# Optimization experiments

Measured on AMD Instinct MI355X. Metric: run time of the kernel, lower is better.

Reference implementation:

```python
import jax, jax.numpy as jnp
import numpy as np

N_NODES = 50000
N_EDGES = 800000
D_FEAT = 128
HIDDEN = 128
BERT_DIM = 768
BATCH = 4096
MAX_ENT = 20
COMB = BERT_DIM + HIDDEN  # 896


def setup_inputs() -> dict:
    key = jax.random.key(0)
    ks = jax.random.split(key, 12)
    article_bert_embeddings = jax.random.normal(ks[0], (BATCH, BERT_DIM), dtype=jnp.float32)
    x = jax.random.normal(ks[1], (N_NODES, D_FEAT), dtype=jnp.float32)
    edge_index = jax.random.randint(ks[2], (2, N_EDGES), 0, N_NODES, dtype=jnp.int64)
    entity_map = jax.random.randint(ks[3], (BATCH, MAX_ENT), 0, N_NODES, dtype=jnp.int64)
    pad = jax.random.uniform(ks[4], (BATCH, MAX_ENT)) < 0.3
    entity_map = jnp.where(pad, jnp.int64(-1), entity_map)
    s = 1.0 / np.sqrt(D_FEAT)
    W1 = jax.random.normal(ks[5], (D_FEAT, HIDDEN), dtype=jnp.float32) * s
    b1 = jnp.zeros((HIDDEN,), dtype=jnp.float32)
    W2 = jax.random.normal(ks[6], (HIDDEN, HIDDEN), dtype=jnp.float32) * (1.0 / np.sqrt(HIDDEN))
    b2 = jnp.zeros((HIDDEN,), dtype=jnp.float32)
    fc1_w = jax.random.normal(ks[7], (COMB, COMB // 2), dtype=jnp.float32) * (1.0 / np.sqrt(COMB))
    fc1_b = jnp.zeros((COMB // 2,), dtype=jnp.float32)
    fc2_w = jax.random.normal(ks[8], (COMB // 2, 1), dtype=jnp.float32) * (1.0 / np.sqrt(COMB // 2))
    fc2_b = jnp.zeros((1,), dtype=jnp.float32)
    return dict(article_bert_embeddings=article_bert_embeddings, x=x,
                edge_index=edge_index, entity_map=entity_map,
                W1=W1, b1=b1, W2=W2, b2=b2,
                fc1_w=fc1_w, fc1_b=fc1_b, fc2_w=fc2_w, fc2_b=fc2_b)


def _gcn_norm(edge_index, n_nodes):
    # add self loops (PyG GCNConv default) and compute symmetric normalization
    loops = jnp.arange(n_nodes, dtype=edge_index.dtype)
    src = jnp.concatenate([edge_index[0], loops])
    dst = jnp.concatenate([edge_index[1], loops])
    deg = jax.ops.segment_sum(jnp.ones_like(dst, dtype=jnp.float32), dst, num_segments=n_nodes)
    dinv = jnp.where(deg > 0, jax.lax.rsqrt(deg), 0.0)
    norm = dinv[src] * dinv[dst]  # [E+N]
    return src, dst, norm


def _gcn_conv(h, W, b, src, dst, norm, n_nodes):
    h = h @ W                                   # [N, H] transform first (cheaper)
    msg = h[src] * norm[:, None]                # [E+N, H] gather
    out = jax.ops.segment_sum(msg, dst, num_segments=n_nodes)
    return out + b


def reference(article_bert_embeddings, x, edge_index, entity_map,
              W1, b1, W2, b2, fc1_w, fc1_b, fc2_w, fc2_b):
    n = x.shape[0]
    src, dst, norm = _gcn_norm(edge_index, n)
    # GNN (dropout in eval mode = identity)
    h = jax.nn.relu(_gcn_conv(x, W1, b1, src, dst, norm, n))
    h = jax.nn.relu(_gcn_conv(h, W2, b2, src, dst, norm, n))
    # ragged mean over entity lists (-1 = padding), fully vectorized
    mask = entity_map >= 0                           # [B, M]
    safe_ids = jnp.where(mask, entity_map, 0)
    gathered = h[safe_ids] * mask[..., None]         # [B, M, H]
    cnt = jnp.maximum(mask.sum(axis=1, keepdims=True).astype(h.dtype), 1.0)
    batch_gnn = gathered.sum(axis=1) / cnt           # [B, H]; rows w/ no entities stay 0
    combined = jnp.concatenate([article_bert_embeddings, batch_gnn], axis=1)
    z = jax.nn.relu(combined @ fc1_w + fc1_b)
    logits = z @ fc2_w + fc2_b
    return jax.nn.sigmoid(logits)
```

## Files before the change

### kernel.cpp

```cpp
#include <hip/hip_runtime.h>
#include <math.h>

typedef __bf16 bf16_t;
typedef __bf16 bfrag8 __attribute__((ext_vector_type(8)));
typedef float  facc4  __attribute__((ext_vector_type(4)));
typedef float  f32x2  __attribute__((ext_vector_type(2)));

#define NBUCK 512
#define BCAP  4096

__device__ inline unsigned short f2b(float x) {
    unsigned int u = __float_as_uint(x);
    unsigned int r = (u + 0x7fffu + ((u >> 16) & 1u)) >> 16;
    return (unsigned short)r;
}
__device__ inline unsigned int pack2(float lo, float hi) {
    return (unsigned int)f2b(lo) | ((unsigned int)f2b(hi) << 16);
}
__device__ inline float blo(unsigned int q) { return __uint_as_float(q << 16); }
__device__ inline float bhi(unsigned int q) { return __uint_as_float(q & 0xffff0000u); }

#if __has_builtin(__builtin_amdgcn_cvt_pk_f32_fp8) && __has_builtin(__builtin_amdgcn_cvt_pk_fp8_f32)
#define HW_FP8 1
#endif

__device__ inline f32x2 fp8pair_dec(unsigned short v) {
#ifdef HW_FP8
    return __builtin_amdgcn_cvt_pk_f32_fp8((int)(unsigned int)v, false);
#else
    f32x2 r;
    unsigned char b0 = (unsigned char)(v & 0xff), b1 = (unsigned char)(v >> 8);
    {
        int e = (b0 >> 3) & 0xf, m = b0 & 7;
        float mag = e ? ldexpf(8.f + m, e - 10) : ldexpf((float)m, -9);
        r.x = (b0 & 0x80) ? -mag : mag;
    }
    {
        int e = (b1 >> 3) & 0xf, m = b1 & 7;
        float mag = e ? ldexpf(8.f + m, e - 10) : ldexpf((float)m, -9);
        r.y = (b1 & 0x80) ? -mag : mag;
    }
    return r;
#endif
}
__device__ inline unsigned char fp8_enc(float x) {
#ifdef HW_FP8
    return (unsigned char)(__builtin_amdgcn_cvt_pk_fp8_f32(x, x, 0, false) & 0xff);
#else
    unsigned char s = (x < 0.f) ? 0x80 : 0;
    float ax = fabsf(x);
    if (!(ax > 0.f)) return s;
    if (ax >= 448.f) return s | 0x7e;
    if (ax < 0.015625f) {
        int q = (int)rintf(ax * 512.f);
        return s | (unsigned char)q;
    }
    int e; float m = frexpf(ax, &e);
    int q = (int)rintf(m * 16.f);
    int E = e - 1;
    if (q == 16) { q = 8; ++E; }
    if (E > 8) return s | 0x7e;
    return s | (unsigned char)(((E + 7) << 3) | (q - 8));
#endif
}

__device__ inline int bucket_of(int d, int N) {
    return (int)(((long long)d * NBUCK) / N);
}

__global__ __launch_bounds__(256) void k_bin2(const int* __restrict__ src,
                                              const int* __restrict__ dst,
                                              int* __restrict__ bcnt,
                                              unsigned int* __restrict__ ebuf,
                                              int E, int N) {
    __shared__ unsigned int sorted[4096];
    __shared__ int hist[NBUCK];
    __shared__ int lstart[NBUCK];
    __shared__ int gbase[NBUCK];
    __shared__ int sm[256];
    int tid = threadIdx.x;
    int base = blockIdx.x * 4096;
    int cnt = min(4096, E - base);
    hist[tid] = 0; hist[tid + 256] = 0;
    __syncthreads();
    unsigned int mye[16]; int myb[16];
#pragma unroll
    for (int i = 0; i < 16; ++i) {
        int idx = i * 256 + tid;
        myb[i] = -1;
        if (idx < cnt) {
            int e = base + idx;
            int s = src[e], d = dst[e];
            mye[i] = ((unsigned int)s << 16) | (unsigned int)d;
            int b = bucket_of(d, N);
            myb[i] = b;
            atomicAdd(&hist[b], 1);
        }
    }
    __syncthreads();
    int p0 = hist[2 * tid], p1 = hist[2 * tid + 1];
    sm[tid] = p0 + p1;
    __syncthreads();
    for (int off = 1; off < 256; off <<= 1) {
        int x = (tid >= off) ? sm[tid - off] : 0;
        __syncthreads();
        sm[tid] += x;
        __syncthreads();
    }
    int excl = sm[tid] - (p0 + p1);
    lstart[2 * tid] = excl;
    lstart[2 * tid + 1] = excl + p0;
    __syncthreads();
    hist[tid] = lstart[tid]; hist[tid + 256] = lstart[tid + 256];
    __syncthreads();
#pragma unroll
    for (int i = 0; i < 16; ++i) {
        if (myb[i] >= 0) {
            int pos = atomicAdd(&hist[myb[i]], 1);
            sorted[pos] = mye[i];
        }
    }
    __syncthreads();
    for (int b = tid; b < NBUCK; b += 256) {
        int c = hist[b] - lstart[b];
        gbase[b] = (c > 0) ? atomicAdd(&bcnt[b], c) : 0;
    }
    __syncthreads();
    for (int idx = tid; idx < cnt; idx += 256) {
        unsigned int v = sorted[idx];
        int b = bucket_of((int)(v & 0xffffu), N);
        ebuf[(size_t)b * BCAP + gbase[b] + (idx - lstart[b])] = v;
    }
}

__global__ void k_bscan(const int* __restrict__ bcnt, int* __restrict__ bstart,
                        int* __restrict__ offs, int N, int E) {
    __shared__ int sm[256];
    int t = threadIdx.x;
    int v0 = bcnt[2 * t], v1 = bcnt[2 * t + 1];
    sm[t] = v0 + v1;
    __syncthreads();
    for (int off = 1; off < 256; off <<= 1) {
        int x = (t >= off) ? sm[t - off] : 0;
        __syncthreads();
        sm[t] += x;
        __syncthreads();
    }
    int excl = sm[t] - (v0 + v1);
    bstart[2 * t] = excl;
    bstart[2 * t + 1] = excl + v0;
    if (t == 0) offs[N] = E;
}

__global__ __launch_bounds__(256) void k_build2(const unsigned int* __restrict__ ebuf,
                                                const int* __restrict__ bcnt,
                                                const int* __restrict__ bstart,
                                                int* __restrict__ offs,
                                                float* __restrict__ dinv,
                                                unsigned short* __restrict__ csr, int N) {
    __shared__ unsigned short seg[BCAP];
    __shared__ int cnt_l[128];
    __shared__ int scan_l[128];
    __shared__ int curs[128];
    int b = blockIdx.x, tid = threadIdx.x;
    int lo = (int)(((long long)b * N + NBUCK - 1) / NBUCK);
    int cnt = bcnt[b];
    int base = bstart[b];
    int nrange = (int)(((long long)(b + 1) * N + NBUCK - 1) / NBUCK) - lo;
    if (tid < 128) cnt_l[tid] = 0;
    __syncthreads();
    for (int i = tid; i < cnt; i += 256) {
        unsigned int v = ebuf[(size_t)b * BCAP + i];
        atomicAdd(&cnt_l[(int)(v & 0xffffu) - lo], 1);
    }
    __syncthreads();
    if (tid < 128) scan_l[tid] = cnt_l[tid];
    __syncthreads();
    for (int off = 1; off < 128; off <<= 1) {
        int x = 0;
        if (tid < 128 && tid >= off) x = scan_l[tid - off];
        __syncthreads();
        if (tid < 128) scan_l[tid] += x;
        __syncthreads();
    }
    if (tid < 128) {
        int excl = scan_l[tid] - cnt_l[tid];
        curs[tid] = excl;
        if (tid < nrange) {
            offs[lo + tid] = base + excl;
            dinv[lo + tid] = rsqrtf((float)(cnt_l[tid] + 1));
        }
    }
    __syncthreads();
    for (int i = tid; i < cnt; i += 256) {
        unsigned int v = ebuf[(size_t)b * BCAP + i];
        int d = (int)(v & 0xffffu) - lo;
        int p = atomicAdd(&curs[d], 1);
        seg[p] = (unsigned short)(v >> 16);
    }
    __syncthreads();
    for (int i = tid; i < cnt; i += 256) csr[base + i] = seg[i];
}

__global__ void k_cvt(const float* __restrict__ in, unsigned int* __restrict__ outb, int n8) {
    int i = blockIdx.x * 256 + threadIdx.x;
    if (i >= n8) return;
    const float4* p = (const float4*)in + (size_t)i * 2;
    float4 a = p[0], b = p[1];
    uint4 o;
    o.x = pack2(a.x, a.y);
    o.y = pack2(a.z, a.w);
    o.z = pack2(b.x, b.y);
    o.w = pack2(b.z, b.w);
    ((uint4*)outb)[i] = o;
}

__global__ void k_prepw_s(const float* __restrict__ W1, unsigned short* __restrict__ w1t,
                          const float* __restrict__ W2, unsigned short* __restrict__ w2t) {
    int i = blockIdx.x * 256 + threadIdx.x;
    if (i >= 32768) return;
    const float* W = (i < 16384) ? W1 : W2;
    unsigned short* Wt = (i < 16384) ? w1t : w2t;
    int idx = i & 16383;
    int n = idx >> 7, k = idx & 127;
    Wt[idx] = f2b(W[k * 128 + n]);
}

__global__ __launch_bounds__(256) void k_tpose(const float* __restrict__ Wf,
                                               unsigned short* __restrict__ fwt) {
    __shared__ float tile[64][65];
    int n0 = blockIdx.x * 64, k0 = blockIdx.y * 64;
#pragma unroll
    for (int i = 0; i < 16; ++i) {
        int idx = i * 256 + threadIdx.x;
        int r = idx >> 6, c = idx & 63;
        tile[r][c] = Wf[(size_t)(k0 + r) * 448 + n0 + c];
    }
    __syncthreads();
#pragma unroll
    for (int i = 0; i < 16; ++i) {
        int idx = i * 256 + threadIdx.x;
        int c = idx >> 6, r = idx & 63;
        fwt[(size_t)(n0 + c) * 896 + k0 + r] = f2b(tile[r][c]);
    }
}

__global__ __launch_bounds__(256) void k_gemm_f32a(const float* __restrict__ A,
                                                   const bf16_t* __restrict__ Bt,
                                                   const float* __restrict__ rs,
                                                   unsigned char* __restrict__ out8, int M) {
    __shared__ bf16_t As[64 * 136];
    __shared__ bf16_t Bs[128 * 136];
    int t = threadIdx.x;
    int wave = t >> 6, lane = t & 63, quad = lane >> 4, l16 = lane & 15;
    int r0 = blockIdx.x * 64;
#pragma unroll
    for (int i = 0; i < 4; ++i) {
        int chunk = t + i * 256;
        int row = chunk >> 4, c8 = (chunk & 15) << 3;
        int gr = r0 + row;
        float4 a0 = make_float4(0.f, 0.f, 0.f, 0.f), a1 = a0;
        if (gr < M) {
            a0 = *(const float4*)&A[(size_t)gr * 128 + c8];
            a1 = *(const float4*)&A[(size_t)gr * 128 + c8 + 4];
        }
        *(uint4*)&As[row * 136 + c8] =
            make_uint4(pack2(a0.x, a0.y), pack2(a0.z, a0.w),
                       pack2(a1.x, a1.y), pack2(a1.z, a1.w));
    }
#pragma unroll
    for (int i = 0; i < 8; ++i) {
        int chunk = t + i * 256;
        int row = chunk >> 4, c8 = (chunk & 15) << 3;
        *(uint4*)&Bs[row * 136 + c8] = *(const uint4*)&Bt[row * 128 + c8];
    }
    __syncthreads();

    facc4 acc[8];
#pragma unroll
    for (int nt = 0; nt < 8; ++nt) acc[nt] = (facc4){0.f, 0.f, 0.f, 0.f};
    int arow = (wave << 4) + l16;
#pragma unroll
    for (int ks = 0; ks < 4; ++ks) {
        int kk = ks * 32 + quad * 8;
        bfrag8 af = *(const bfrag8*)&As[arow * 136 + kk];
#pragma unroll
        for (int nt = 0; nt < 8; ++nt) {
            bfrag8 bf = *(const bfrag8*)&Bs[(nt * 16 + l16) * 136 + kk];
            acc[nt] = __builtin_amdgcn_mfma_f32_16x16x32_bf16(af, bf, acc[nt], 0, 0, 0);
        }
    }
    __syncthreads();
    unsigned char* f8t = (unsigned char*)As;
    int wrow0 = (wave << 4) + quad * 4;
#pragma unroll
    for (int r = 0; r < 4; ++r) {
        int row = wrow0 + r;
        float sc = rs[min(r0 + row, M - 1)];
#pragma unroll
        for (int nt = 0; nt < 8; ++nt)
            f8t[row * 128 + nt * 16 + l16] = fp8_enc(acc[nt][r] * sc);
    }
    __syncthreads();
#pragma unroll
    for (int i = 0; i < 2; ++i) {
        int idx = t + i * 256;
        int row = idx >> 3, cc = (idx & 7) << 4;
        int gr = r0 + row;
        if (gr < M) *(uint4*)&out8[(size_t)gr * 128 + cc] = *(const uint4*)&f8t[row * 128 + cc];
    }
}

__global__ __launch_bounds__(256) void k_gemm_nn128(const bf16_t* __restrict__ A,
                                                    const bf16_t* __restrict__ Bt,
                                                    const float* __restrict__ rs,
                                                    unsigned char* __restrict__ out8, int M) {
    __shared__ bf16_t As[64 * 136];
    __shared__ bf16_t Bs[128 * 136];
    int t = threadIdx.x;
    int wave = t >> 6, lane = t & 63, quad = lane >> 4, l16 = lane & 15;
    int r0 = blockIdx.x * 64;
#pragma unroll
    for (int i = 0; i < 4; ++i) {
        int chunk = t + i * 256;
        int row = chunk >> 4, c8 = (chunk & 15) << 3;
        int gr = r0 + row;
        uint4 v = make_uint4(0u, 0u, 0u, 0u);
        if (gr < M) v = *(const uint4*)&A[(size_t)gr * 128 + c8];
        *(uint4*)&As[row * 136 + c8] = v;
    }
#pragma unroll
    for (int i = 0; i < 8; ++i) {
        int chunk = t + i * 256;
        int row = chunk >> 4, c8 = (chunk & 15) << 3;
        *(uint4*)&Bs[row * 136 + c8] = *(const uint4*)&Bt[row * 128 + c8];
    }
    __syncthreads();

    facc4 acc[8];
#pragma unroll
    for (int nt = 0; nt < 8; ++nt) acc[nt] = (facc4){0.f, 0.f, 0.f, 0.f};
    int arow = (wave << 4) + l16;
#pragma unroll
    for (int ks = 0; ks < 4; ++ks) {
        int kk = ks * 32 + quad * 8;
        bfrag8 af = *(const bfrag8*)&As[arow * 136 + kk];
#pragma unroll
        for (int nt = 0; nt < 8; ++nt) {
            bfrag8 bf = *(const bfrag8*)&Bs[(nt * 16 + l16) * 136 + kk];
            acc[nt] = __builtin_amdgcn_mfma_f32_16x16x32_bf16(af, bf, acc[nt], 0, 0, 0);
        }
    }
    __syncthreads();
    unsigned char* f8t = (unsigned char*)As;
    int wrow0 = (wave << 4) + quad * 4;
#pragma unroll
    for (int r = 0; r < 4; ++r) {
        int row = wrow0 + r;
        float sc = rs[min(r0 + row, M - 1)];
#pragma unroll
        for (int nt = 0; nt < 8; ++nt)
            f8t[row * 128 + nt * 16 + l16] = fp8_enc(acc[nt][r] * sc);
    }
    __syncthreads();
#pragma unroll
    for (int i = 0; i < 2; ++i) {
        int idx = t + i * 256;
        int row = idx >> 3, cc = (idx & 7) << 4;
        int gr = r0 + row;
        if (gr < M) *(uint4*)&out8[(size_t)gr * 128 + cc] = *(const uint4*)&f8t[row * 128 + cc];
    }
}

__global__ __launch_bounds__(256) void k_agg_b(const unsigned short* __restrict__ hx8,
                                               const unsigned short* __restrict__ csr,
                                               const int* __restrict__ offs,
                                               const float* __restrict__ dinv,
                                               const float* __restrict__ bias,
                                               unsigned int* __restrict__ out, int N) {
    int node = blockIdx.x * 4 + (threadIdx.x >> 6);
    int lane = threadIdx.x & 63;
    if (node >= N) return;
    float di = dinv[node];
    f32x2 sf = fp8pair_dec(hx8[(size_t)node * 64 + lane]);
    float acc0 = sf.x, acc1 = sf.y;
    int s0 = offs[node], s1 = offs[node + 1];
    for (int base = s0; base < s1; base += 64) {
        int nloc = min(64, s1 - base);
        int en = 0;
        if (lane < nloc) en = (int)csr[base + lane];
        int j = 0;
        for (; j + 16 <= nloc; j += 16) {
            int sid[16]; unsigned short g[16];
#pragma unroll
            for (int u = 0; u < 16; ++u) sid[u] = __shfl(en, j + u, 64);
#pragma unroll
            for (int u = 0; u < 16; ++u) g[u] = hx8[(size_t)sid[u] * 64 + lane];
#pragma unroll
            for (int u = 0; u < 16; ++u) { f32x2 d = fp8pair_dec(g[u]); acc0 += d.x; acc1 += d.y; }
        }
        for (; j + 4 <= nloc; j += 4) {
            int sid[4]; unsigned short g[4];
#pragma unroll
            for (int u = 0; u < 4; ++u) sid[u] = __shfl(en, j + u, 64);
#pragma unroll
            for (int u = 0; u < 4; ++u) g[u] = hx8[(size_t)sid[u] * 64 + lane];
#pragma unroll
            for (int u = 0; u < 4; ++u) { f32x2 d = fp8pair_dec(g[u]); acc0 += d.x; acc1 += d.y; }
        }
        for (; j < nloc; ++j) {
            int srcn = __shfl(en, j, 64);
            f32x2 d = fp8pair_dec(hx8[(size_t)srcn * 64 + lane]);
            acc0 += d.x; acc1 += d.y;
        }
    }
    float2 bb = *(const float2*)&bias[lane * 2];
    float v0 = fmaxf(acc0 * di + bb.x, 0.f);
    float v1 = fmaxf(acc1 * di + bb.y, 0.f);
    out[(size_t)node * 64 + lane] = pack2(v0, v1);
}

__global__ __launch_bounds__(256) void k_pool_b(const unsigned int* __restrict__ h,
                                                const int* __restrict__ ent,
                                                unsigned int* __restrict__ out) {
    int r = blockIdx.x * 4 + (threadIdx.x >> 6);
    int lane = threadIdx.x & 63;
    float a0 = 0.f, a1 = 0.f;
    int cnt = 0;
#pragma unroll
    for (int m = 0; m < 20; ++m) {
        int id = ent[r * 20 + m];
        if (id >= 0) {
            unsigned int q = h[(size_t)id * 64 + lane];
            a0 += blo(q); a1 += bhi(q); cnt++;
        }
    }
    float inv = 1.f / (float)max(cnt, 1);
    out[(size_t)r * 64 + lane] = pack2(a0 * inv, a1 * inv);
}

__global__ __launch_bounds__(256) void k_mlp1_mfma(const bf16_t* __restrict__ bertb,
                                                   const bf16_t* __restrict__ gnnb,
                                                   const bf16_t* __restrict__ fwt,
                                                   const float* __restrict__ fb,
                                                   float* __restrict__ z) {
    __shared__ bf16_t As[64 * 136];
    __shared__ bf16_t Bs[64 * 136];
    int t = threadIdx.x;
    int wave = t >> 6, lane = t & 63, quad = lane >> 4, l16 = lane & 15;
    int r0 = blockIdx.x * 64, c0 = blockIdx.y * 64;
    facc4 acc[4];
#pragma unroll
    for (int nt = 0; nt < 4; ++nt) acc[nt] = (facc4){0.f, 0.f, 0.f, 0.f};

    for (int ks = 0; ks < 7; ++ks) {
#pragma unroll
        for (int i = 0; i < 4; ++i) {
            int chunk = t + i * 256;
            int row = chunk >> 4, c8 = (chunk & 15) << 3;
            int gr = r0 + row;
            const bf16_t* srcp = (ks < 6) ? &bertb[(size_t)gr * 768 + ks * 128 + c8]
                                          : &gnnb[(size_t)gr * 128 + c8];
            *(uint4*)&As[row * 136 + c8] = *(const uint4*)srcp;
        }
#pragma unroll
        for (int i = 0; i < 4; ++i) {
            int chunk = t + i * 256;
            int row = chunk >> 4, c8 = (chunk & 15) << 3;
            *(uint4*)&Bs[row * 136 + c8] =
                *(const uint4*)&fwt[(size_t)(c0 + row) * 896 + ks * 128 + c8];
        }
        __syncthreads();
        int arow = (wave << 4) + l16;
#pragma unroll
        for (int sub = 0; sub < 4; ++sub) {
            int kk = sub * 32 + quad * 8;
            bfrag8 af = *(const bfrag8*)&As[arow * 136 + kk];
#pragma unroll
            for (int nt = 0; nt < 4; ++nt) {
                bfrag8 bf = *(const bfrag8*)&Bs[(nt * 16 + l16) * 136 + kk];
                acc[nt] = __builtin_amdgcn_mfma_f32_16x16x32_bf16(af, bf, acc[nt], 0, 0, 0);
            }
        }
        __syncthreads();
    }
    int rbase = r0 + (wave << 4) + quad * 4;
#pragma unroll
    for (int nt = 0; nt < 4; ++nt) {
        int col = c0 + nt * 16 + l16;
        float bb = fb[col];
#pragma unroll
        for (int r = 0; r < 4; ++r)
            z[(size_t)(rbase + r) * 448 + col] = fmaxf(acc[nt][r] + bb, 0.f);
    }
}

__global__ __launch_bounds__(256) void k_mlp2(const float* __restrict__ z,
                                              const float* __restrict__ w,
                                              const float* __restrict__ b,
                                              float* __restrict__ out) {
    int r = blockIdx.x * 4 + (threadIdx.x >> 6);
    int lane = threadIdx.x & 63;
    float acc = 0.f;
#pragma unroll
    for (int i = 0; i < 7; ++i) {
        int c = lane + i * 64;
        acc += z[(size_t)r * 448 + c] * w[c];
    }
#pragma unroll
    for (int off = 32; off > 0; off >>= 1) acc += __shfl_down(acc, off, 64);
    if (lane == 0) {
        float lg = acc + b[0];
        out[r] = 1.f / (1.f + expf(-lg));
    }
}

extern "C" void kernel_launch(void* const* d_in, const int* in_sizes, int n_in,
                              void* d_out, int out_size, void* d_ws, size_t ws_size,
                              hipStream_t stream) {
    const float* bert = (const float*)d_in[0];
    const float* x    = (const float*)d_in[1];
    const int*   ei   = (const int*)d_in[2];
    const int*   ent  = (const int*)d_in[3];
    const float* W1   = (const float*)d_in[4];
    const float* b1   = (const float*)d_in[5];
    const float* W2   = (const float*)d_in[6];
    const float* b2   = (const float*)d_in[7];
    const float* fc1w = (const float*)d_in[8];
    const float* fc1b = (const float*)d_in[9];
    const float* fc2w = (const float*)d_in[10];
    const float* fc2b = (const float*)d_in[11];
    float* out = (float*)d_out;

    const int N = in_sizes[1] / 128;
    const int E = in_sizes[2] / 2;
    const int B = in_sizes[0] / 768;

    const int* srcv = ei;
    const int* dstv = ei + E;

    char* wsp = (char*)d_ws;
    size_t off = 0;
    auto alloc = [&](size_t bytes) -> void* {
        void* p = wsp + off;
        off += (bytes + 255) & ~(size_t)255;
        return p;
    };
    float* dinv   = (float*)alloc((size_t)N * 4);
    int*   offs   = (int*)alloc((size_t)(N + 1) * 4);
    int*   bcnt   = (int*)alloc(NBUCK * 4);
    int*   bstart = (int*)alloc(NBUCK * 4);
    unsigned int*   ebuf  = (unsigned int*)alloc((size_t)NBUCK * BCAP * 4);
    unsigned short* csr16 = (unsigned short*)alloc((size_t)E * 2);
    bf16_t* bertb = (bf16_t*)alloc((size_t)B * 768 * 2);
    bf16_t* w1t   = (bf16_t*)alloc(128 * 128 * 2);
    bf16_t* w2t   = (bf16_t*)alloc(128 * 128 * 2);
    bf16_t* fwt   = (bf16_t*)alloc((size_t)896 * 448 * 2);
    unsigned char* g8buf = (unsigned char*)alloc((size_t)N * 128);
    bf16_t* hbuf  = (bf16_t*)alloc((size_t)N * 128 * 2);
    bf16_t* gnnb  = (bf16_t*)alloc((size_t)B * 128 * 2);
    float* zbuf   = (float*)alloc((size_t)B * 448 * 4);
    (void)ws_size; (void)n_in; (void)out_size;

    hipMemsetAsync(bcnt, 0, NBUCK * 4, stream);

    k_bin2  <<<(E + 4095) / 4096, 256, 0, stream>>>(srcv, dstv, bcnt, ebuf, E, N);
    k_bscan <<<1, 256, 0, stream>>>(bcnt, bstart, offs, N, E);
    k_build2<<<NBUCK, 256, 0, stream>>>(ebuf, bcnt, bstart, offs, dinv, csr16, N);

    int nb8 = B * 768 / 8;
    k_cvt<<<(nb8 + 255) / 256, 256, 0, stream>>>(bert, (unsigned int*)bertb, nb8);
    k_prepw_s<<<(32768 + 255) / 256, 256, 0, stream>>>(W1, (unsigned short*)w1t,
                                                       W2, (unsigned short*)w2t);
    k_tpose<<<dim3(448 / 64, 896 / 64), 256, 0, stream>>>(fc1w, (unsigned short*)fwt);

    int gb = (N + 63) / 64;
    k_gemm_f32a<<<gb, 256, 0, stream>>>(x, w1t, dinv, g8buf, N);
    k_agg_b<<<(N + 3) / 4, 256, 0, stream>>>((const unsigned short*)g8buf, csr16, offs, dinv, b1,
                                             (unsigned int*)hbuf, N);
    k_gemm_nn128<<<gb, 256, 0, stream>>>(hbuf, w2t, dinv, g8buf, N);
    k_agg_b<<<(N + 3) / 4, 256, 0, stream>>>((const unsigned short*)g8buf, csr16, offs, dinv, b2,
                                             (unsigned int*)hbuf, N);
    k_pool_b<<<B / 4, 256, 0, stream>>>((const unsigned int*)hbuf, ent, (unsigned int*)gnnb);
    k_mlp1_mfma<<<dim3(B / 64, 7), 256, 0, stream>>>(bertb, gnnb, fwt, fc1b, zbuf);
    k_mlp2<<<B / 4, 256, 0, stream>>>(zbuf, fc2w, fc2b, out);
}
```

Measured before the change: 222.0 us.

## Merge prep kernels, fold bucket scan into build, fuse fc2 into fc1 epilogue

Merges the bf16 conversion, weight transposes and zero-initialisation into one multi-role prep kernel, which replaces a memset and three launches. The single-block bucket scan is dropped; each build block instead reduces the preceding bucket counts itself. The fc2 dot product moves into the fc1 MFMA epilogue as a shuffle reduction plus atomicAdd into per-row logits, which removes the z intermediate buffer and the mlp2 pass. A small sigmoid kernel finishes the output. The cost is redundant prefix work in every build block and atomics with a nondeterministic summation order.

```diff
diff --git a/kernel.cpp b/kernel.cpp
--- a/kernel.cpp
+++ b/kernel.cpp
@@ -133,40 +133,31 @@
     }
 }
 
-__global__ void k_bscan(const int* __restrict__ bcnt, int* __restrict__ bstart,
-                        int* __restrict__ offs, int N, int E) {
-    __shared__ int sm[256];
-    int t = threadIdx.x;
-    int v0 = bcnt[2 * t], v1 = bcnt[2 * t + 1];
-    sm[t] = v0 + v1;
-    __syncthreads();
-    for (int off = 1; off < 256; off <<= 1) {
-        int x = (t >= off) ? sm[t - off] : 0;
-        __syncthreads();
-        sm[t] += x;
-        __syncthreads();
-    }
-    int excl = sm[t] - (v0 + v1);
-    bstart[2 * t] = excl;
-    bstart[2 * t + 1] = excl + v0;
-    if (t == 0) offs[N] = E;
-}
-
 __global__ __launch_bounds__(256) void k_build2(const unsigned int* __restrict__ ebuf,
                                                 const int* __restrict__ bcnt,
-                                                const int* __restrict__ bstart,
                                                 int* __restrict__ offs,
                                                 float* __restrict__ dinv,
-                                                unsigned short* __restrict__ csr, int N) {
+                                                unsigned short* __restrict__ csr,
+                                                int N, int E) {
     __shared__ unsigned short seg[BCAP];
     __shared__ int cnt_l[128];
     __shared__ int scan_l[128];
     __shared__ int curs[128];
+    __shared__ int smr[256];
     int b = blockIdx.x, tid = threadIdx.x;
+    int part = 0;
+    for (int j = tid; j < b; j += 256) part += bcnt[j];
+    smr[tid] = part;
+    __syncthreads();
+    for (int off = 128; off > 0; off >>= 1) {
+        if (tid < off) smr[tid] += smr[tid + off];
+        __syncthreads();
+    }
+    int base = smr[0];
     int lo = (int)(((long long)b * N + NBUCK - 1) / NBUCK);
     int cnt = bcnt[b];
-    int base = bstart[b];
     int nrange = (int)(((long long)(b + 1) * N + NBUCK - 1) / NBUCK) - lo;
+    if (b == 0 && tid == 0) offs[N] = E;
     if (tid < 128) cnt_l[tid] = 0;
     __syncthreads();
     for (int i = tid; i < cnt; i += 256) {
@@ -202,47 +193,63 @@
     for (int i = tid; i < cnt; i += 256) csr[base + i] = seg[i];
 }
 
-__global__ void k_cvt(const float* __restrict__ in, unsigned int* __restrict__ outb, int n8) {
-    int i = blockIdx.x * 256 + threadIdx.x;
-    if (i >= n8) return;
-    const float4* p = (const float4*)in + (size_t)i * 2;
-    float4 a = p[0], b = p[1];
-    uint4 o;
-    o.x = pack2(a.x, a.y);
-    o.y = pack2(a.z, a.w);
-    o.z = pack2(b.x, b.y);
-    o.w = pack2(b.z, b.w);
-    ((uint4*)outb)[i] = o;
-}
-
-__global__ void k_prepw_s(const float* __restrict__ W1, unsigned short* __restrict__ w1t,
-                          const float* __restrict__ W2, unsigned short* __restrict__ w2t) {
-    int i = blockIdx.x * 256 + threadIdx.x;
-    if (i >= 32768) return;
-    const float* W = (i < 16384) ? W1 : W2;
-    unsigned short* Wt = (i < 16384) ? w1t : w2t;
-    int idx = i & 16383;
-    int n = idx >> 7, k = idx & 127;
-    Wt[idx] = f2b(W[k * 128 + n]);
-}
-
-__global__ __launch_bounds__(256) void k_tpose(const float* __restrict__ Wf,
-                                               unsigned short* __restrict__ fwt) {
+__global__ __launch_bounds__(256) void k_prep(const float* __restrict__ bert,
+                                              unsigned int* __restrict__ bertb, int n8,
+                                              const float* __restrict__ W1,
+                                              unsigned short* __restrict__ w1t,
+                                              const float* __restrict__ W2,
+                                              unsigned short* __restrict__ w2t,
+                                              const float* __restrict__ Wf,
+                                              unsigned short* __restrict__ fwt,
+                                              int* __restrict__ bcnt,
+                                              float* __restrict__ logacc) {
     __shared__ float tile[64][65];
-    int n0 = blockIdx.x * 64, k0 = blockIdx.y * 64;
-#pragma unroll
-    for (int i = 0; i < 16; ++i) {
-        int idx = i * 256 + threadIdx.x;
-        int r = idx >> 6, c = idx & 63;
-        tile[r][c] = Wf[(size_t)(k0 + r) * 448 + n0 + c];
-    }
-    __syncthreads();
-#pragma unroll
-    for (int i = 0; i < 16; ++i) {
-        int idx = i * 256 + threadIdx.x;
-        int c = idx >> 6, r = idx & 63;
-        fwt[(size_t)(n0 + c) * 896 + k0 + r] = f2b(tile[r][c]);
-    }
+    int ncvt = (n8 + 255) / 256;
+    int bb = blockIdx.x, tid = threadIdx.x;
+    if (bb < ncvt) {
+        int i = bb * 256 + tid;
+        if (i >= n8) return;
+        const float4* p = (const float4*)bert + (size_t)i * 2;
+        float4 a = p[0], b = p[1];
+        uint4 o;
+        o.x = pack2(a.x, a.y);
+        o.y = pack2(a.z, a.w);
+        o.z = pack2(b.x, b.y);
+        o.w = pack2(b.z, b.w);
+        ((uint4*)bertb)[i] = o;
+        return;
+    }
+    bb -= ncvt;
+    if (bb < 128) {
+        int i = bb * 256 + tid;
+        const float* W = (i < 16384) ? W1 : W2;
+        unsigned short* Wt = (i < 16384) ? w1t : w2t;
+        int idx = i & 16383;
+        int n = idx >> 7, k = idx & 127;
+        Wt[idx] = f2b(W[k * 128 + n]);
+        return;
+    }
+    bb -= 128;
+    if (bb < 98) {
+        int n0 = (bb % 7) * 64, k0 = (bb / 7) * 64;
+#pragma unroll
+        for (int i = 0; i < 16; ++i) {
+            int idx = i * 256 + tid;
+            int r = idx >> 6, c = idx & 63;
+            tile[r][c] = Wf[(size_t)(k0 + r) * 448 + n0 + c];
+        }
+        __syncthreads();
+#pragma unroll
+        for (int i = 0; i < 16; ++i) {
+            int idx = i * 256 + tid;
+            int c = idx >> 6, r = idx & 63;
+            fwt[(size_t)(n0 + c) * 896 + k0 + r] = f2b(tile[r][c]);
+        }
+        return;
+    }
+    if (tid < 256) { bcnt[tid] = 0; bcnt[tid + 256] = 0; }
+#pragma unroll
+    for (int i = 0; i < 16; ++i) logacc[i * 256 + tid] = 0.f;
 }
 
 __global__ __launch_bounds__(256) void k_gemm_f32a(const float* __restrict__ A,
@@ -443,7 +450,8 @@
                                                    const bf16_t* __restrict__ gnnb,
                                                    const bf16_t* __restrict__ fwt,
                                                    const float* __restrict__ fb,
-                                                   float* __restrict__ z) {
+                                                   const float* __restrict__ w2,
+                                                   float* __restrict__ logacc) {
     __shared__ bf16_t As[64 * 136];
     __shared__ bf16_t Bs[64 * 136];
     int t = threadIdx.x;
@@ -485,34 +493,31 @@
         __syncthreads();
     }
     int rbase = r0 + (wave << 4) + quad * 4;
+    float part[4] = {0.f, 0.f, 0.f, 0.f};
 #pragma unroll
     for (int nt = 0; nt < 4; ++nt) {
         int col = c0 + nt * 16 + l16;
         float bb = fb[col];
+        float ww = w2[col];
 #pragma unroll
         for (int r = 0; r < 4; ++r)
-            z[(size_t)(rbase + r) * 448 + col] = fmaxf(acc[nt][r] + bb, 0.f);
-    }
-}
-
-__global__ __launch_bounds__(256) void k_mlp2(const float* __restrict__ z,
-                                              const float* __restrict__ w,
-                                              const float* __restrict__ b,
-                                              float* __restrict__ out) {
-    int r = blockIdx.x * 4 + (threadIdx.x >> 6);
-    int lane = threadIdx.x & 63;
-    float acc = 0.f;
-#pragma unroll
-    for (int i = 0; i < 7; ++i) {
-        int c = lane + i * 64;
-        acc += z[(size_t)r * 448 + c] * w[c];
-    }
-#pragma unroll
-    for (int off = 32; off > 0; off >>= 1) acc += __shfl_down(acc, off, 64);
-    if (lane == 0) {
-        float lg = acc + b[0];
-        out[r] = 1.f / (1.f + expf(-lg));
-    }
+            part[r] += fmaxf(acc[nt][r] + bb, 0.f) * ww;
+    }
+#pragma unroll
+    for (int m = 8; m >= 1; m >>= 1) {
+#pragma unroll
+        for (int r = 0; r < 4; ++r) part[r] += __shfl_xor(part[r], m, 64);
+    }
+    if (l16 == 0) {
+#pragma unroll
+        for (int r = 0; r < 4; ++r) atomicAdd(&logacc[rbase + r], part[r]);
+    }
+}
+
+__global__ void k_sig(const float* __restrict__ logacc, const float* __restrict__ b,
+                      float* __restrict__ out, int B) {
+    int i = blockIdx.x * 256 + threadIdx.x;
+    if (i < B) out[i] = 1.f / (1.f + expf(-(logacc[i] + b[0])));
 }
 
 extern "C" void kernel_launch(void* const* d_in, const int* in_sizes, int n_in,
@@ -549,7 +554,7 @@
     float* dinv   = (float*)alloc((size_t)N * 4);
     int*   offs   = (int*)alloc((size_t)(N + 1) * 4);
     int*   bcnt   = (int*)alloc(NBUCK * 4);
-    int*   bstart = (int*)alloc(NBUCK * 4);
+    float* logacc = (float*)alloc((size_t)B * 4);
     unsigned int*   ebuf  = (unsigned int*)alloc((size_t)NBUCK * BCAP * 4);
     unsigned short* csr16 = (unsigned short*)alloc((size_t)E * 2);
     bf16_t* bertb = (bf16_t*)alloc((size_t)B * 768 * 2);
@@ -559,20 +564,16 @@
     unsigned char* g8buf = (unsigned char*)alloc((size_t)N * 128);
     bf16_t* hbuf  = (bf16_t*)alloc((size_t)N * 128 * 2);
     bf16_t* gnnb  = (bf16_t*)alloc((size_t)B * 128 * 2);
-    float* zbuf   = (float*)alloc((size_t)B * 448 * 4);
     (void)ws_size; (void)n_in; (void)out_size;
 
-    hipMemsetAsync(bcnt, 0, NBUCK * 4, stream);
-
+    int nb8 = B * 768 / 8;
+    int ncvt = (nb8 + 255) / 256;
+    int nprep = ncvt + 128 + 98 + 1;
+    k_prep<<<nprep, 256, 0, stream>>>(bert, (unsigned int*)bertb, nb8,
+                                      W1, (unsigned short*)w1t, W2, (unsigned short*)w2t,
+                                      fc1w, (unsigned short*)fwt, bcnt, logacc);
     k_bin2  <<<(E + 4095) / 4096, 256, 0, stream>>>(srcv, dstv, bcnt, ebuf, E, N);
-    k_bscan <<<1, 256, 0, stream>>>(bcnt, bstart, offs, N, E);
-    k_build2<<<NBUCK, 256, 0, stream>>>(ebuf, bcnt, bstart, offs, dinv, csr16, N);
-
-    int nb8 = B * 768 / 8;
-    k_cvt<<<(nb8 + 255) / 256, 256, 0, stream>>>(bert, (unsigned int*)bertb, nb8);
-    k_prepw_s<<<(32768 + 255) / 256, 256, 0, stream>>>(W1, (unsigned short*)w1t,
-                                                       W2, (unsigned short*)w2t);
-    k_tpose<<<dim3(448 / 64, 896 / 64), 256, 0, stream>>>(fc1w, (unsigned short*)fwt);
+    k_build2<<<NBUCK, 256, 0, stream>>>(ebuf, bcnt, offs, dinv, csr16, N, E);
 
     int gb = (N + 63) / 64;
     k_gemm_f32a<<<gb, 256, 0, stream>>>(x, w1t, dinv, g8buf, N);
@@ -582,6 +583,6 @@
     k_agg_b<<<(N + 3) / 4, 256, 0, stream>>>((const unsigned short*)g8buf, csr16, offs, dinv, b2,
                                              (unsigned int*)hbuf, N);
     k_pool_b<<<B / 4, 256, 0, stream>>>((const unsigned int*)hbuf, ent, (unsigned int*)gnnb);
-    k_mlp1_mfma<<<dim3(B / 64, 7), 256, 0, stream>>>(bertb, gnnb, fwt, fc1b, zbuf);
-    k_mlp2<<<B / 4, 256, 0, stream>>>(zbuf, fc2w, fc2b, out);
-}
+    k_mlp1_mfma<<<dim3(B / 64, 7), 256, 0, stream>>>(bertb, gnnb, fwt, fc1b, fc2w, logacc);
+    k_sig<<<(B + 255) / 256, 256, 0, stream>>>(logacc, fc2b, out, B);
+}
```

After: 217.6 us. 2.0% less time.
